# Optimization experiments

Hardware: AMD Instinct MI355X
Metric: run time of the kernel (lower is better)

Reference implementation:

```python
import jax, jax.numpy as jnp
import numpy as np

B = 128        # graph pairs per batch
NPG = 512      # nodes per graph (equal-size graphs -> dense batch is a reshape)
D = 64         # input feature dim
DEG = 16       # avg degree
FILTERS = [64, 32, 16]
RDIM = 10      # resize_dim
CCH = 8        # conv channels per similarity image
MLP = [32, 16, 8, 4, 1]


def _make_edges(rng, n_graphs, npg, deg):
    E = n_graphs * npg * deg
    off = np.repeat(np.arange(n_graphs, dtype=np.int64) * npg, npg * deg)
    src = rng.integers(0, npg, E) + off
    dst = rng.integers(0, npg, E) + off
    return jnp.asarray(np.stack([src, dst]), dtype=jnp.int32)


def setup_inputs() -> dict:
    key = jax.random.key(0)
    ks = jax.random.split(key, 40)
    rng = np.random.default_rng(0)
    N = B * NPG
    inp = {}
    inp['x_i'] = jax.random.normal(ks[0], (N, D), jnp.float32)
    inp['x_j'] = jax.random.normal(ks[1], (N, D), jnp.float32)
    # GCN weights
    dims = [D] + FILTERS
    k = 2
    for li in range(3):
        fi, fo = dims[li], dims[li + 1]
        inp[f'gcn_w{li}'] = jax.random.normal(ks[k], (fi, fo), jnp.float32) / np.sqrt(fi); k += 1
        inp[f'gcn_b{li}'] = jnp.zeros((fo,), jnp.float32)
    # Conv filters: one Conv2d(1->CCH, 3x3, SAME) per GNN layer, OIHW kernels
    for li in range(3):
        inp[f'conv_w{li}'] = jax.random.normal(ks[k], (CCH, 1, 3, 3), jnp.float32) / 3.0; k += 1
        inp[f'conv_b{li}'] = jnp.zeros((CCH,), jnp.float32)
    # MLP (Linear-ReLU stack) + scoring layer
    mdims = [3 * CCH * RDIM * RDIM] + MLP
    for li in range(len(MLP)):
        fi, fo = mdims[li], mdims[li + 1]
        inp[f'mlp_w{li}'] = jax.random.normal(ks[k], (fi, fo), jnp.float32) / np.sqrt(fi); k += 1
        inp[f'mlp_b{li}'] = jnp.zeros((fo,), jnp.float32)
    inp['score_w'] = jax.random.normal(ks[k], (1, 1), jnp.float32); k += 1
    inp['score_b'] = jnp.zeros((1,), jnp.float32)
    # Graph structure (int constants)
    inp['edge_index_i'] = _make_edges(rng, B, NPG, DEG)
    inp['edge_index_j'] = _make_edges(rng, B, NPG, DEG)
    batch = jnp.asarray(np.repeat(np.arange(B, dtype=np.int64), NPG), dtype=jnp.int32)
    inp['batch_i'] = batch
    inp['batch_j'] = batch
    return inp


def _gcn(x, ei, w, b):
    # PyG GCNConv: A_hat = D^-1/2 (A + I) D^-1/2 ; out = A_hat (x W) + b
    src, dst = ei[0], ei[1]
    n = x.shape[0]
    xw = x @ w
    deg = jax.ops.segment_sum(jnp.ones(ei.shape[1], xw.dtype), dst, num_segments=n) + 1.0
    inv = jax.lax.rsqrt(deg)
    msg = xw[src] * (inv[src] * inv[dst])[:, None]
    agg = jax.ops.segment_sum(msg, dst, num_segments=n)
    return agg + xw * (inv * inv)[:, None] + b


def _forward(x_i, x_j, gcn_w0, gcn_b0, gcn_w1, gcn_b1, gcn_w2, gcn_b2,
             conv_w0, conv_b0, conv_w1, conv_b1, conv_w2, conv_b2,
             mlp_w0, mlp_b0, mlp_w1, mlp_b1, mlp_w2, mlp_b2, mlp_w3, mlp_b3, mlp_w4, mlp_b4,
             score_w, score_b, edge_index_i, edge_index_j):
    gws = [(gcn_w0, gcn_b0), (gcn_w1, gcn_b1), (gcn_w2, gcn_b2)]
    cvs = [(conv_w0, conv_b0), (conv_w1, conv_b1), (conv_w2, conv_b2)]
    embs = []
    for li, (w, b) in enumerate(gws):
        x_i = _gcn(x_i, edge_index_i, w, b)
        x_j = _gcn(x_j, edge_index_j, w, b)
        if li != len(gws) - 1:  # activation + dropout (eval mode -> identity)
            x_i = jax.nn.relu(x_i)
            x_j = jax.nn.relu(x_j)
        h_i = x_i.reshape(B, NPG, -1)  # to_dense_batch (equal-size graphs)
        h_j = x_j.reshape(B, NPG, -1)
        sim = jnp.einsum('bnd,bmd->bnm', h_i, h_j)  # [B, NPG, NPG]
        simr = jax.image.resize(sim, (B, RDIM, RDIM), method='bilinear', antialias=False)
        cw, cb = cvs[li]
        y = jax.lax.conv_general_dilated(simr[:, None], cw, (1, 1), 'SAME')
        y = jax.nn.relu(y + cb[None, :, None, None])  # [B, CCH, RDIM, RDIM]
        embs.append(y.reshape(B, -1))
    feat = jnp.concatenate(embs, axis=1)  # [B, 3*CCH*RDIM*RDIM]
    for w, b in [(mlp_w0, mlp_b0), (mlp_w1, mlp_b1), (mlp_w2, mlp_b2), (mlp_w3, mlp_b3), (mlp_w4, mlp_b4)]:
        feat = jax.nn.relu(feat @ w + b)
    score = jax.nn.sigmoid(feat @ score_w + score_b)
    return score.reshape(-1)


def reference(x_i, x_j, gcn_w0, gcn_b0, gcn_w1, gcn_b1, gcn_w2, gcn_b2,
              conv_w0, conv_b0, conv_w1, conv_b1, conv_w2, conv_b2,
              mlp_w0, mlp_b0, mlp_w1, mlp_b1, mlp_w2, mlp_b2, mlp_w3, mlp_b3, mlp_w4, mlp_b4,
              score_w, score_b, edge_index_i, edge_index_j, batch_i, batch_j):
    # batch_i/batch_j are implicit in the block layout (equal-size graphs)
    return _forward(x_i, x_j, gcn_w0, gcn_b0, gcn_w1, gcn_b1, gcn_w2, gcn_b2,
                    conv_w0, conv_b0, conv_w1, conv_b1, conv_w2, conv_b2,
                    mlp_w0, mlp_b0, mlp_w1, mlp_b1, mlp_w2, mlp_b2, mlp_w3, mlp_b3, mlp_w4, mlp_b4,
                    score_w, score_b, edge_index_i, edge_index_j)
```

## Files before the change

### kernel.cpp

```cpp
#include <hip/hip_runtime.h>
#include <hip/hip_fp16.h>

typedef float fvec4 __attribute__((ext_vector_type(4)));
typedef int ivec4 __attribute__((ext_vector_type(4)));

#define NN 65536
#define EE 1048576
#define BB 128
#define NPG 512
#define EPG 8192

__device__ __forceinline__ int pkrtz(float a, float b) {
  union { __half2 h; int i; } u; u.h = __floats2half2_rn(a, b); return u.i;
}
__device__ __forceinline__ float2 up2(int v) {
  union { int i; __half2 h; } u; u.i = v; return __half22float2(u.h);
}

#define ACCQ(SA, SB, w) { float2 f_; \
  f_ = up2((w)[0]); (SA)[0] += f_.x; (SA)[1] += f_.y; \
  f_ = up2((w)[1]); (SA)[2] += f_.x; (SA)[3] += f_.y; \
  f_ = up2((w)[2]); (SB)[0] += f_.x; (SB)[1] += f_.y; \
  f_ = up2((w)[3]); (SB)[2] += f_.x; (SB)[3] += f_.y; }

__global__ __launch_bounds__(512)
void k_all(const float* __restrict__ x_i, const float* __restrict__ x_j,
           const float* __restrict__ gw0, const float* __restrict__ gb0,
           const float* __restrict__ gw1, const float* __restrict__ gb1,
           const float* __restrict__ gw2, const float* __restrict__ gb2,
           const int* __restrict__ ei, const int* __restrict__ ej,
           float* __restrict__ hs0, float* __restrict__ hs1, float* __restrict__ hs2) {
  __shared__ ivec4 bufA[NPG * 4];
  __shared__ ivec4 bufB[NPG * 4];
  __shared__ unsigned short sids[EPG];
  __shared__ int cnt[NPG];
  __shared__ int posb[NPG];
  __shared__ int nodeOf[NPG];
  __shared__ int bins[64];
  __shared__ int binpos[64];
  __shared__ int wsum[8];
  unsigned short* const dsts = reinterpret_cast<unsigned short*>(bufA);

  const int side = blockIdx.x >> 7;
  const int g = blockIdx.x & 127;
  const float* __restrict__ x = side ? x_j : x_i;
  const int* __restrict__ eidx = side ? ej : ei;
  const int v = threadIdx.x;
  const int base = g * NPG;
  const int ebase = g * EPG;

  cnt[v] = 0;
  if (v < 64) bins[v] = 0;
  __syncthreads();
  for (int k = v; k < EPG; k += 512) {
    int d = eidx[EE + ebase + k] - base;
    dsts[k] = (unsigned short)d;
    atomicAdd(&cnt[d], 1);
  }
  __syncthreads();

  const int count = cnt[v];
  const int deg = count > 63 ? 63 : count;
  atomicAdd(&bins[deg], 1);
  int xa = count;
  const int lane = v & 63;
#pragma unroll
  for (int d = 1; d < 64; d <<= 1) {
    int y = __shfl_up(xa, d, 64);
    if (lane >= d) xa += y;
  }
  const int wid = v >> 6;
  if (lane == 63) wsum[wid] = xa;
  __syncthreads();
  if (v < 64) {
    if (v == 0) {
      int a = 0;
#pragma unroll
      for (int i = 0; i < 8; ++i) { int tv = wsum[i]; wsum[i] = a; a += tv; }
    }
    int c = bins[v];
    int xb = c;
#pragma unroll
    for (int d = 1; d < 64; d <<= 1) {
      int y = __shfl_up(xb, d, 64);
      if (v >= d) xb += y;
    }
    binpos[v] = xb - c;
  }
  __syncthreads();
  const int start_v = xa - count + wsum[wid];
  posb[v] = start_v;
  {
    int rank = atomicAdd(&binpos[deg], 1);
    nodeOf[rank] = v;
  }
  __syncthreads();

  for (int k = v; k < EPG; k += 512) {
    int lv = eidx[ebase + k] - base;
    int p = atomicAdd(&posb[dsts[k]], 1);
    sids[p] = (unsigned short)((lv << 2) | ((lv >> 1) & 3));
  }
  __syncthreads();

  const int node = nodeOf[v];
  const int ncount = cnt[node];
  const int nstart = posb[node] - ncount;
  const float inv_v = rsqrtf((float)ncount + 1.0f);
  const int myKey = (node << 2) | ((node >> 1) & 3);

  constexpr int srows[20] = {25, 26, 76, 77, 127, 128, 178, 179, 229, 230,
                             281, 282, 332, 333, 383, 384, 434, 435, 485, 486};
  int slot = -1;
#pragma unroll
  for (int i = 0; i < 20; ++i)
    if (node == srows[i]) slot = i;
  const int hb = (side * BB + g) * 20;

  fvec4 a0[16];
#pragma unroll
  for (int q = 0; q < 16; ++q) a0[q] = fvec4{0.f, 0.f, 0.f, 0.f};
  {
    const fvec4* xv = reinterpret_cast<const fvec4*>(x + (size_t)(base + node) * 64);
#pragma unroll 1
    for (int k16 = 0; k16 < 4; ++k16) {
      fvec4 xq[4];
#pragma unroll
      for (int u = 0; u < 4; ++u) xq[u] = xv[4 * k16 + u];
#pragma unroll
      for (int u = 0; u < 4; ++u) {
#pragma unroll
        for (int j = 0; j < 4; ++j) {
          const float xk = xq[u][j];
          const fvec4* wr = reinterpret_cast<const fvec4*>(gw0 + (size_t)(16 * k16 + 4 * u + j) * 64);
#pragma unroll
          for (int q = 0; q < 16; ++q) a0[q] += xk * wr[q];
        }
      }
    }
  }

  fvec4 s[8];
#pragma unroll
  for (int q = 0; q < 8; ++q) s[q] = a0[q] * inv_v;
#pragma unroll
  for (int q_ = 0; q_ < 4; ++q_) {
    ivec4 w_;
    w_[0] = pkrtz(s[2 * q_][0], s[2 * q_][1]);
    w_[1] = pkrtz(s[2 * q_][2], s[2 * q_][3]);
    w_[2] = pkrtz(s[2 * q_ + 1][0], s[2 * q_ + 1][1]);
    w_[3] = pkrtz(s[2 * q_ + 1][2], s[2 * q_ + 1][3]);
    bufA[myKey ^ q_] = w_;
  }
  __syncthreads();

  {
    const int end = nstart + ncount;
    for (int e = nstart; e < end; ++e) {
      const int K = sids[e];
      const ivec4 w0 = bufA[K], w1 = bufA[K ^ 1], w2 = bufA[K ^ 2], w3 = bufA[K ^ 3];
      ACCQ(s[0], s[1], w0) ACCQ(s[2], s[3], w1) ACCQ(s[4], s[5], w2) ACCQ(s[6], s[7], w3)
    }
  }

  fvec4 sB[8];
#pragma unroll
  for (int q = 0; q < 8; ++q) sB[q] = a0[8 + q] * inv_v;
#pragma unroll
  for (int q_ = 0; q_ < 4; ++q_) {
    ivec4 w_;
    w_[0] = pkrtz(sB[2 * q_][0], sB[2 * q_][1]);
    w_[1] = pkrtz(sB[2 * q_][2], sB[2 * q_][3]);
    w_[2] = pkrtz(sB[2 * q_ + 1][0], sB[2 * q_ + 1][1]);
    w_[3] = pkrtz(sB[2 * q_ + 1][2], sB[2 * q_ + 1][3]);
    bufB[myKey ^ q_] = w_;
  }

  fvec4 y1[8];
#pragma unroll
  for (int p = 0; p < 8; ++p) y1[p] = fvec4{0.f, 0.f, 0.f, 0.f};
  {
    const fvec4* gb0v = reinterpret_cast<const fvec4*>(gb0);
    fvec4* hp = reinterpret_cast<fvec4*>(hs0 + ((size_t)hb + slot) * 64);
#pragma unroll
    for (int q = 0; q < 8; ++q) {
      fvec4 o = s[q] * inv_v + gb0v[q];
#pragma unroll
      for (int j = 0; j < 4; ++j) o[j] = fmaxf(o[j], 0.f);
      if (slot >= 0) hp[q] = o;
#pragma unroll
      for (int j = 0; j < 4; ++j) {
        const float hf = o[j];
        const fvec4* wr = reinterpret_cast<const fvec4*>(gw1 + (size_t)(q * 4 + j) * 32);
#pragma unroll
        for (int p = 0; p < 8; ++p) y1[p] += hf * wr[p];
      }
    }
  }
  __syncthreads();

  {
    const int end = nstart + ncount;
    for (int e = nstart; e < end; ++e) {
      const int K = sids[e];
      const ivec4 w0 = bufB[K], w1 = bufB[K ^ 1], w2 = bufB[K ^ 2], w3 = bufB[K ^ 3];
      ACCQ(sB[0], sB[1], w0) ACCQ(sB[2], sB[3], w1) ACCQ(sB[4], sB[5], w2) ACCQ(sB[6], sB[7], w3)
    }
  }
  {
    const fvec4* gb0v = reinterpret_cast<const fvec4*>(gb0);
    fvec4* hp = reinterpret_cast<fvec4*>(hs0 + ((size_t)hb + slot) * 64);
#pragma unroll
    for (int q = 0; q < 8; ++q) {
      fvec4 o = sB[q] * inv_v + gb0v[8 + q];
#pragma unroll
      for (int j = 0; j < 4; ++j) o[j] = fmaxf(o[j], 0.f);
      if (slot >= 0) hp[8 + q] = o;
#pragma unroll
      for (int j = 0; j < 4; ++j) {
        const float hf = o[j];
        const fvec4* wr = reinterpret_cast<const fvec4*>(gw1 + (size_t)((8 + q) * 4 + j) * 32);
#pragma unroll
        for (int p = 0; p < 8; ++p) y1[p] += hf * wr[p];
      }
    }
  }

  fvec4 s1[8];
#pragma unroll
  for (int q = 0; q < 8; ++q) s1[q] = y1[q] * inv_v;
#pragma unroll
  for (int q_ = 0; q_ < 4; ++q_) {
    ivec4 w_;
    w_[0] = pkrtz(s1[2 * q_][0], s1[2 * q_][1]);
    w_[1] = pkrtz(s1[2 * q_][2], s1[2 * q_][3]);
    w_[2] = pkrtz(s1[2 * q_ + 1][0], s1[2 * q_ + 1][1]);
    w_[3] = pkrtz(s1[2 * q_ + 1][2], s1[2 * q_ + 1][3]);
    bufA[myKey ^ q_] = w_;
  }
  __syncthreads();

  {
    const int end = nstart + ncount;
    for (int e = nstart; e < end; ++e) {
      const int K = sids[e];
      const ivec4 w0 = bufA[K], w1 = bufA[K ^ 1], w2 = bufA[K ^ 2], w3 = bufA[K ^ 3];
      ACCQ(s1[0], s1[1], w0) ACCQ(s1[2], s1[3], w1) ACCQ(s1[4], s1[5], w2) ACCQ(s1[6], s1[7], w3)
    }
  }
  fvec4 y2[4];
#pragma unroll
  for (int p = 0; p < 4; ++p) y2[p] = fvec4{0.f, 0.f, 0.f, 0.f};
  {
    const fvec4* gb1v = reinterpret_cast<const fvec4*>(gb1);
    fvec4* hp = reinterpret_cast<fvec4*>(hs1 + ((size_t)hb + slot) * 32);
#pragma unroll
    for (int q = 0; q < 8; ++q) {
      fvec4 o = s1[q] * inv_v + gb1v[q];
#pragma unroll
      for (int j = 0; j < 4; ++j) o[j] = fmaxf(o[j], 0.f);
      if (slot >= 0) hp[q] = o;
#pragma unroll
      for (int j = 0; j < 4; ++j) {
        const float hf = o[j];
        const fvec4* wr = reinterpret_cast<const fvec4*>(gw2 + (size_t)(q * 4 + j) * 16);
#pragma unroll
        for (int p = 0; p < 4; ++p) y2[p] += hf * wr[p];
      }
    }
  }

  fvec4 s2[4];
#pragma unroll
  for (int q = 0; q < 4; ++q) s2[q] = y2[q] * inv_v;
  {
    ivec4 w0, w1;
    w0[0] = pkrtz(s2[0][0], s2[0][1]); w0[1] = pkrtz(s2[0][2], s2[0][3]);
    w0[2] = pkrtz(s2[1][0], s2[1][1]); w0[3] = pkrtz(s2[1][2], s2[1][3]);
    w1[0] = pkrtz(s2[2][0], s2[2][1]); w1[1] = pkrtz(s2[2][2], s2[2][3]);
    w1[2] = pkrtz(s2[3][0], s2[3][1]); w1[3] = pkrtz(s2[3][2], s2[3][3]);
    bufB[myKey] = w0;
    bufB[myKey ^ 1] = w1;
  }
  __syncthreads();

  if (slot >= 0) {
    const int end = nstart + ncount;
    for (int e = nstart; e < end; ++e) {
      const int K = sids[e];
      const ivec4 w0 = bufB[K], w1 = bufB[K ^ 1];
      ACCQ(s2[0], s2[1], w0) ACCQ(s2[2], s2[3], w1)
    }
    const fvec4* gb2v = reinterpret_cast<const fvec4*>(gb2);
    fvec4* hp = reinterpret_cast<fvec4*>(hs2 + ((size_t)hb + slot) * 16);
#pragma unroll
    for (int q = 0; q < 4; ++q) hp[q] = s2[q] * inv_v + gb2v[q];
  }
}

__global__ __launch_bounds__(256) void k_head(const float* __restrict__ hs0, const float* __restrict__ hs1,
                                              const float* __restrict__ hs2,
                                              const float* __restrict__ cw0, const float* __restrict__ cb0,
                                              const float* __restrict__ cw1, const float* __restrict__ cb1,
                                              const float* __restrict__ cw2, const float* __restrict__ cb2,
                                              const float* __restrict__ mw0, const float* __restrict__ mb0,
                                              const float* __restrict__ mw1, const float* __restrict__ mb1,
                                              const float* __restrict__ mw2, const float* __restrict__ mb2,
                                              const float* __restrict__ mw3, const float* __restrict__ mb3,
                                              const float* __restrict__ mw4, const float* __restrict__ mb4,
                                              const float* __restrict__ sw, const float* __restrict__ sb,
                                              float* __restrict__ out) {
  __shared__ float hi[2240];
  __shared__ float hj[2240];
  __shared__ float sim[400];
  __shared__ float simr[100];
  __shared__ float feat[2400];
  __shared__ float red[256];
  __shared__ float mbuf[60];
  const int b = blockIdx.x, t = threadIdx.x;

  for (int k = t; k < 1280; k += 256) {
    hi[k] = hs0[(size_t)(0 * BB + b) * 1280 + k];
    hj[k] = hs0[(size_t)(1 * BB + b) * 1280 + k];
  }
  for (int k = t; k < 640; k += 256) {
    hi[1280 + k] = hs1[(size_t)(0 * BB + b) * 640 + k];
    hj[1280 + k] = hs1[(size_t)(1 * BB + b) * 640 + k];
  }
  for (int k = t; k < 320; k += 256) {
    hi[1920 + k] = hs2[(size_t)(0 * BB + b) * 320 + k];
    hj[1920 + k] = hs2[(size_t)(1 * BB + b) * 320 + k];
  }
  __syncthreads();

  const int Fs[3] = {64, 32, 16};
  const int HOFF[3] = {0, 1280, 1920};
  const float* CW[3] = {cw0, cw1, cw2};
  const float* CB[3] = {cb0, cb1, cb2};

  for (int li = 0; li < 3; ++li) {
    const int F = Fs[li];
    const float* Hi = hi + HOFF[li];
    const float* Hj = hj + HOFF[li];
    for (int p = t; p < 400; p += 256) {
      int r = p / 20, cq = p % 20;
      float a = 0.0f;
      for (int d = 0; d < F; ++d) a += Hi[r * F + d] * Hj[cq * F + d];
      sim[p] = a;
    }
    __syncthreads();
    if (t < 100) {
      int oy = t / 10, ox = t % 10;
      float cy = (oy + 0.5f) * (512.0f / 10.0f) - 0.5f;
      float cx = (ox + 0.5f) * (512.0f / 10.0f) - 0.5f;
      float fy = cy - floorf(cy);
      float fx = cx - floorf(cx);
      int r0 = 2 * oy, c0 = 2 * ox;
      float s00 = sim[r0 * 20 + c0], s01 = sim[r0 * 20 + c0 + 1];
      float s10 = sim[(r0 + 1) * 20 + c0], s11 = sim[(r0 + 1) * 20 + c0 + 1];
      simr[t] = (1.0f - fy) * ((1.0f - fx) * s00 + fx * s01) + fy * ((1.0f - fx) * s10 + fx * s11);
    }
    __syncthreads();
    const float* cw = CW[li];
    const float* cb = CB[li];
    for (int idx = t; idx < 800; idx += 256) {
      int cch = idx / 100, rem = idx % 100, y = rem / 10, x = rem % 10;
      float a = cb[cch];
#pragma unroll
      for (int ky = 0; ky < 3; ++ky) {
#pragma unroll
        for (int kx = 0; kx < 3; ++kx) {
          int iy = y + ky - 1, ix = x + kx - 1;
          if (iy >= 0 && iy < 10 && ix >= 0 && ix < 10)
            a += cw[cch * 9 + ky * 3 + kx] * simr[iy * 10 + ix];
        }
      }
      feat[li * 800 + idx] = fmaxf(a, 0.0f);
    }
    __syncthreads();
  }

  {
    int f = t & 31, part = t >> 5;
    float a = 0.0f;
    int k0 = part * 300;
    for (int k = k0; k < k0 + 300; ++k) a += feat[k] * mw0[k * 32 + f];
    red[t] = a;
    __syncthreads();
    if (t < 32) {
      float s = mb0[t];
#pragma unroll
      for (int p = 0; p < 8; ++p) s += red[p * 32 + t];
      mbuf[t] = fmaxf(s, 0.0f);
    }
    __syncthreads();
  }
  if (t < 16) {
    float s = mb1[t];
    for (int k = 0; k < 32; ++k) s += mbuf[k] * mw1[k * 16 + t];
    mbuf[32 + t] = fmaxf(s, 0.0f);
  }
  __syncthreads();
  if (t < 8) {
    float s = mb2[t];
    for (int k = 0; k < 16; ++k) s += mbuf[32 + k] * mw2[k * 8 + t];
    mbuf[48 + t] = fmaxf(s, 0.0f);
  }
  __syncthreads();
  if (t < 4) {
    float s = mb3[t];
    for (int k = 0; k < 8; ++k) s += mbuf[48 + k] * mw3[k * 4 + t];
    mbuf[56 + t] = fmaxf(s, 0.0f);
  }
  __syncthreads();
  if (t == 0) {
    float s = mb4[0];
    for (int k = 0; k < 4; ++k) s += mbuf[56 + k] * mw4[k];
    s = fmaxf(s, 0.0f);
    float z = s * sw[0] + sb[0];
    out[b] = 1.0f / (1.0f + expf(-z));
  }
}

extern "C" void kernel_launch(void* const* d_in, const int* in_sizes, int n_in,
                              void* d_out, int out_size, void* d_ws, size_t ws_size,
                              hipStream_t stream) {
  (void)in_sizes; (void)n_in; (void)out_size; (void)ws_size;
  const float* x_i = (const float*)d_in[0];
  const float* x_j = (const float*)d_in[1];
  const float* gw0 = (const float*)d_in[2];
  const float* gb0 = (const float*)d_in[3];
  const float* gw1 = (const float*)d_in[4];
  const float* gb1 = (const float*)d_in[5];
  const float* gw2 = (const float*)d_in[6];
  const float* gb2 = (const float*)d_in[7];
  const float* cw0 = (const float*)d_in[8];
  const float* cb0 = (const float*)d_in[9];
  const float* cw1 = (const float*)d_in[10];
  const float* cb1 = (const float*)d_in[11];
  const float* cw2 = (const float*)d_in[12];
  const float* cb2 = (const float*)d_in[13];
  const float* mw0 = (const float*)d_in[14];
  const float* mb0 = (const float*)d_in[15];
  const float* mw1 = (const float*)d_in[16];
  const float* mb1 = (const float*)d_in[17];
  const float* mw2 = (const float*)d_in[18];
  const float* mb2 = (const float*)d_in[19];
  const float* mw3 = (const float*)d_in[20];
  const float* mb3 = (const float*)d_in[21];
  const float* mw4 = (const float*)d_in[22];
  const float* mb4 = (const float*)d_in[23];
  const float* scw = (const float*)d_in[24];
  const float* scb = (const float*)d_in[25];
  const int* ei = (const int*)d_in[26];
  const int* ej = (const int*)d_in[27];
  float* out = (float*)d_out;

  char* p = (char*)d_ws;
  auto take = [&](size_t bytes) {
    char* r = p;
    p += (bytes + 255) & ~(size_t)255;
    return r;
  };
  float* hs0 = (float*)take((size_t)2 * BB * 20 * 64 * 4);
  float* hs1 = (float*)take((size_t)2 * BB * 20 * 32 * 4);
  float* hs2 = (float*)take((size_t)2 * BB * 20 * 16 * 4);

  k_all<<<2 * BB, 512, 0, stream>>>(x_i, x_j, gw0, gb0, gw1, gb1, gw2, gb2,
                                    ei, ej, hs0, hs1, hs2);
  k_head<<<BB, 256, 0, stream>>>(hs0, hs1, hs2, cw0, cb0, cw1, cb1, cw2, cb2,
                                 mw0, mb0, mw1, mb1, mw2, mb2, mw3, mb3, mw4, mb4,
                                 scw, scb, out);
}
```

Before: 131.7 us.

## Merge layer-0 half buffers into one sync, unroll gathers, spread final-layer rows

```diff
diff --git a/kernel.cpp b/kernel.cpp
--- a/kernel.cpp
+++ b/kernel.cpp
@@ -22,6 +22,21 @@
   f_ = up2((w)[1]); (SA)[2] += f_.x; (SA)[3] += f_.y; \
   f_ = up2((w)[2]); (SB)[0] += f_.x; (SB)[1] += f_.y; \
   f_ = up2((w)[3]); (SB)[2] += f_.x; (SB)[3] += f_.y; }
+
+#define GATHER32(buf, S, startE, countE) { \
+  int e_ = (startE); const int end_ = (startE) + (countE); \
+  for (; e_ + 2 <= end_; e_ += 2) { \
+    const int Ka_ = sids[e_], Kb_ = sids[e_ + 1]; \
+    const ivec4 a0_ = (buf)[Ka_], a1_ = (buf)[Ka_ ^ 1], a2_ = (buf)[Ka_ ^ 2], a3_ = (buf)[Ka_ ^ 3]; \
+    const ivec4 b0_ = (buf)[Kb_], b1_ = (buf)[Kb_ ^ 1], b2_ = (buf)[Kb_ ^ 2], b3_ = (buf)[Kb_ ^ 3]; \
+    ACCQ((S)[0], (S)[1], a0_) ACCQ((S)[2], (S)[3], a1_) ACCQ((S)[4], (S)[5], a2_) ACCQ((S)[6], (S)[7], a3_) \
+    ACCQ((S)[0], (S)[1], b0_) ACCQ((S)[2], (S)[3], b1_) ACCQ((S)[4], (S)[5], b2_) ACCQ((S)[6], (S)[7], b3_) \
+  } \
+  if (e_ < end_) { \
+    const int Ka_ = sids[e_]; \
+    const ivec4 a0_ = (buf)[Ka_], a1_ = (buf)[Ka_ ^ 1], a2_ = (buf)[Ka_ ^ 2], a3_ = (buf)[Ka_ ^ 3]; \
+    ACCQ((S)[0], (S)[1], a0_) ACCQ((S)[2], (S)[3], a1_) ACCQ((S)[4], (S)[5], a2_) ACCQ((S)[6], (S)[7], a3_) \
+  } }
 
 __global__ __launch_bounds__(512)
 void k_all(const float* __restrict__ x_i, const float* __restrict__ x_j,
@@ -145,36 +160,21 @@
   for (int q = 0; q < 8; ++q) s[q] = a0[q] * inv_v;
 #pragma unroll
   for (int q_ = 0; q_ < 4; ++q_) {
-    ivec4 w_;
-    w_[0] = pkrtz(s[2 * q_][0], s[2 * q_][1]);
-    w_[1] = pkrtz(s[2 * q_][2], s[2 * q_][3]);
-    w_[2] = pkrtz(s[2 * q_ + 1][0], s[2 * q_ + 1][1]);
-    w_[3] = pkrtz(s[2 * q_ + 1][2], s[2 * q_ + 1][3]);
-    bufA[myKey ^ q_] = w_;
-  }
-  __syncthreads();
-
-  {
-    const int end = nstart + ncount;
-    for (int e = nstart; e < end; ++e) {
-      const int K = sids[e];
-      const ivec4 w0 = bufA[K], w1 = bufA[K ^ 1], w2 = bufA[K ^ 2], w3 = bufA[K ^ 3];
-      ACCQ(s[0], s[1], w0) ACCQ(s[2], s[3], w1) ACCQ(s[4], s[5], w2) ACCQ(s[6], s[7], w3)
-    }
-  }
-
-  fvec4 sB[8];
-#pragma unroll
-  for (int q = 0; q < 8; ++q) sB[q] = a0[8 + q] * inv_v;
-#pragma unroll
-  for (int q_ = 0; q_ < 4; ++q_) {
-    ivec4 w_;
-    w_[0] = pkrtz(sB[2 * q_][0], sB[2 * q_][1]);
-    w_[1] = pkrtz(sB[2 * q_][2], sB[2 * q_][3]);
-    w_[2] = pkrtz(sB[2 * q_ + 1][0], sB[2 * q_ + 1][1]);
-    w_[3] = pkrtz(sB[2 * q_ + 1][2], sB[2 * q_ + 1][3]);
-    bufB[myKey ^ q_] = w_;
-  }
+    ivec4 wA, wB;
+    wA[0] = pkrtz(s[2 * q_][0], s[2 * q_][1]);
+    wA[1] = pkrtz(s[2 * q_][2], s[2 * q_][3]);
+    wA[2] = pkrtz(s[2 * q_ + 1][0], s[2 * q_ + 1][1]);
+    wA[3] = pkrtz(s[2 * q_ + 1][2], s[2 * q_ + 1][3]);
+    fvec4 b0 = a0[8 + 2 * q_] * inv_v;
+    fvec4 b1 = a0[8 + 2 * q_ + 1] * inv_v;
+    wB[0] = pkrtz(b0[0], b0[1]); wB[1] = pkrtz(b0[2], b0[3]);
+    wB[2] = pkrtz(b1[0], b1[1]); wB[3] = pkrtz(b1[2], b1[3]);
+    bufA[myKey ^ q_] = wA;
+    bufB[myKey ^ q_] = wB;
+  }
+  __syncthreads();
+
+  GATHER32(bufA, s, nstart, ncount)
 
   fvec4 y1[8];
 #pragma unroll
@@ -197,16 +197,16 @@
       }
     }
   }
-  __syncthreads();
-
-  {
-    const int end = nstart + ncount;
-    for (int e = nstart; e < end; ++e) {
-      const int K = sids[e];
-      const ivec4 w0 = bufB[K], w1 = bufB[K ^ 1], w2 = bufB[K ^ 2], w3 = bufB[K ^ 3];
-      ACCQ(sB[0], sB[1], w0) ACCQ(sB[2], sB[3], w1) ACCQ(sB[4], sB[5], w2) ACCQ(sB[6], sB[7], w3)
-    }
-  }
+
+  fvec4 sB[8];
+#pragma unroll
+  for (int q = 0; q < 8; ++q) sB[q] = fvec4{0.f, 0.f, 0.f, 0.f};
+  {
+    const ivec4 w0 = bufB[myKey], w1 = bufB[myKey ^ 1], w2 = bufB[myKey ^ 2], w3 = bufB[myKey ^ 3];
+    ACCQ(sB[0], sB[1], w0) ACCQ(sB[2], sB[3], w1) ACCQ(sB[4], sB[5], w2) ACCQ(sB[6], sB[7], w3)
+  }
+  GATHER32(bufB, sB, nstart, ncount)
+
   {
     const fvec4* gb0v = reinterpret_cast<const fvec4*>(gb0);
     fvec4* hp = reinterpret_cast<fvec4*>(hs0 + ((size_t)hb + slot) * 64);
@@ -225,6 +225,7 @@
       }
     }
   }
+  __syncthreads();
 
   fvec4 s1[8];
 #pragma unroll
@@ -240,14 +241,8 @@
   }
   __syncthreads();
 
-  {
-    const int end = nstart + ncount;
-    for (int e = nstart; e < end; ++e) {
-      const int K = sids[e];
-      const ivec4 w0 = bufA[K], w1 = bufA[K ^ 1], w2 = bufA[K ^ 2], w3 = bufA[K ^ 3];
-      ACCQ(s1[0], s1[1], w0) ACCQ(s1[2], s1[3], w1) ACCQ(s1[4], s1[5], w2) ACCQ(s1[6], s1[7], w3)
-    }
-  }
+  GATHER32(bufA, s1, nstart, ncount)
+
   fvec4 y2[4];
 #pragma unroll
   for (int p = 0; p < 4; ++p) y2[p] = fvec4{0.f, 0.f, 0.f, 0.f};
@@ -270,31 +265,49 @@
     }
   }
 
-  fvec4 s2[4];
-#pragma unroll
-  for (int q = 0; q < 4; ++q) s2[q] = y2[q] * inv_v;
-  {
+  {
+    fvec4 q0 = y2[0] * inv_v, q1 = y2[1] * inv_v, q2 = y2[2] * inv_v, q3 = y2[3] * inv_v;
     ivec4 w0, w1;
-    w0[0] = pkrtz(s2[0][0], s2[0][1]); w0[1] = pkrtz(s2[0][2], s2[0][3]);
-    w0[2] = pkrtz(s2[1][0], s2[1][1]); w0[3] = pkrtz(s2[1][2], s2[1][3]);
-    w1[0] = pkrtz(s2[2][0], s2[2][1]); w1[1] = pkrtz(s2[2][2], s2[2][3]);
-    w1[2] = pkrtz(s2[3][0], s2[3][1]); w1[3] = pkrtz(s2[3][2], s2[3][3]);
+    w0[0] = pkrtz(q0[0], q0[1]); w0[1] = pkrtz(q0[2], q0[3]);
+    w0[2] = pkrtz(q1[0], q1[1]); w0[3] = pkrtz(q1[2], q1[3]);
+    w1[0] = pkrtz(q2[0], q2[1]); w1[1] = pkrtz(q2[2], q2[3]);
+    w1[2] = pkrtz(q3[0], q3[1]); w1[3] = pkrtz(q3[2], q3[3]);
     bufB[myKey] = w0;
     bufB[myKey ^ 1] = w1;
   }
   __syncthreads();
 
-  if (slot >= 0) {
-    const int end = nstart + ncount;
-    for (int e = nstart; e < end; ++e) {
-      const int K = sids[e];
-      const ivec4 w0 = bufB[K], w1 = bufB[K ^ 1];
+  if (v < 20) {
+    const int n = srows[v];
+    const int ccount = cnt[n];
+    const int cstart = posb[n] - ccount;
+    const float cinv = rsqrtf((float)ccount + 1.0f);
+    const int ckey = (n << 2) | ((n >> 1) & 3);
+    fvec4 s2[4];
+#pragma unroll
+    for (int q = 0; q < 4; ++q) s2[q] = fvec4{0.f, 0.f, 0.f, 0.f};
+    {
+      const ivec4 w0 = bufB[ckey], w1 = bufB[ckey ^ 1];
       ACCQ(s2[0], s2[1], w0) ACCQ(s2[2], s2[3], w1)
     }
+    int e = cstart;
+    const int end = cstart + ccount;
+    for (; e + 2 <= end; e += 2) {
+      const int Ka = sids[e], Kb = sids[e + 1];
+      const ivec4 a0_ = bufB[Ka], a1_ = bufB[Ka ^ 1];
+      const ivec4 b0_ = bufB[Kb], b1_ = bufB[Kb ^ 1];
+      ACCQ(s2[0], s2[1], a0_) ACCQ(s2[2], s2[3], a1_)
+      ACCQ(s2[0], s2[1], b0_) ACCQ(s2[2], s2[3], b1_)
+    }
+    if (e < end) {
+      const int Ka = sids[e];
+      const ivec4 a0_ = bufB[Ka], a1_ = bufB[Ka ^ 1];
+      ACCQ(s2[0], s2[1], a0_) ACCQ(s2[2], s2[3], a1_)
+    }
     const fvec4* gb2v = reinterpret_cast<const fvec4*>(gb2);
-    fvec4* hp = reinterpret_cast<fvec4*>(hs2 + ((size_t)hb + slot) * 16);
-#pragma unroll
-    for (int q = 0; q < 4; ++q) hp[q] = s2[q] * inv_v + gb2v[q];
+    fvec4* hp = reinterpret_cast<fvec4*>(hs2 + ((size_t)hb + v) * 16);
+#pragma unroll
+    for (int q = 0; q < 4; ++q) hp[q] = s2[q] * cinv + gb2v[q];
   }
 }
 
```

Result: no change. 130.3 us (-1.0%).

## Split fused GCN kernel into three per-layer kernels with feature-half blocks

Applied to the files above, without the earlier changes.

```diff
diff --git a/kernel.cpp b/kernel.cpp
--- a/kernel.cpp
+++ b/kernel.cpp
@@ -23,34 +23,42 @@
   f_ = up2((w)[2]); (SB)[0] += f_.x; (SB)[1] += f_.y; \
   f_ = up2((w)[3]); (SB)[2] += f_.x; (SB)[3] += f_.y; }
 
+__device__ __forceinline__ int slot_of(int node) {
+  constexpr int srows[20] = {25, 26, 76, 77, 127, 128, 178, 179, 229, 230,
+                             281, 282, 332, 333, 383, 384, 434, 435, 485, 486};
+  int slot = -1;
+#pragma unroll
+  for (int i = 0; i < 20; ++i)
+    if (node == srows[i]) slot = i;
+  return slot;
+}
+__constant__ int c_srows[20] = {25, 26, 76, 77, 127, 128, 178, 179, 229, 230,
+                                281, 282, 332, 333, 383, 384, 434, 435, 485, 486};
+
 __global__ __launch_bounds__(512)
-void k_all(const float* __restrict__ x_i, const float* __restrict__ x_j,
-           const float* __restrict__ gw0, const float* __restrict__ gb0,
-           const float* __restrict__ gw1, const float* __restrict__ gb1,
-           const float* __restrict__ gw2, const float* __restrict__ gb2,
-           const int* __restrict__ ei, const int* __restrict__ ej,
-           float* __restrict__ hs0, float* __restrict__ hs1, float* __restrict__ hs2) {
-  __shared__ ivec4 bufA[NPG * 4];
-  __shared__ ivec4 bufB[NPG * 4];
+void kA(const float* __restrict__ x_i, const float* __restrict__ x_j,
+        const float* __restrict__ gw0, const float* __restrict__ gb0,
+        const float* __restrict__ gw1,
+        const int* __restrict__ ei, const int* __restrict__ ej,
+        unsigned short* __restrict__ sidsG, unsigned int* __restrict__ packG,
+        float* __restrict__ hs0, unsigned int* __restrict__ y1G) {
+  __shared__ ivec4 buf[NPG * 4];
   __shared__ unsigned short sids[EPG];
   __shared__ int cnt[NPG];
   __shared__ int posb[NPG];
-  __shared__ int nodeOf[NPG];
-  __shared__ int bins[64];
-  __shared__ int binpos[64];
   __shared__ int wsum[8];
-  unsigned short* const dsts = reinterpret_cast<unsigned short*>(bufA);
-
-  const int side = blockIdx.x >> 7;
-  const int g = blockIdx.x & 127;
+  unsigned short* const dsts = reinterpret_cast<unsigned short*>(buf);
+
+  const int bid = blockIdx.x;
+  const int half = bid & 1;
+  const int sg = bid >> 1;
+  const int side = sg >> 7, g = sg & 127;
   const float* __restrict__ x = side ? x_j : x_i;
   const int* __restrict__ eidx = side ? ej : ei;
   const int v = threadIdx.x;
-  const int base = g * NPG;
-  const int ebase = g * EPG;
+  const int base = g * NPG, ebase = g * EPG;
 
   cnt[v] = 0;
-  if (v < 64) bins[v] = 0;
   __syncthreads();
   for (int k = v; k < EPG; k += 512) {
     int d = eidx[EE + ebase + k] - base;
@@ -60,8 +68,6 @@
   __syncthreads();
 
   const int count = cnt[v];
-  const int deg = count > 63 ? 63 : count;
-  atomicAdd(&bins[deg], 1);
   int xa = count;
   const int lane = v & 63;
 #pragma unroll
@@ -72,56 +78,27 @@
   const int wid = v >> 6;
   if (lane == 63) wsum[wid] = xa;
   __syncthreads();
-  if (v < 64) {
-    if (v == 0) {
-      int a = 0;
-#pragma unroll
-      for (int i = 0; i < 8; ++i) { int tv = wsum[i]; wsum[i] = a; a += tv; }
-    }
-    int c = bins[v];
-    int xb = c;
-#pragma unroll
-    for (int d = 1; d < 64; d <<= 1) {
-      int y = __shfl_up(xb, d, 64);
-      if (v >= d) xb += y;
-    }
-    binpos[v] = xb - c;
-  }
-  __syncthreads();
-  const int start_v = xa - count + wsum[wid];
-  posb[v] = start_v;
-  {
-    int rank = atomicAdd(&binpos[deg], 1);
-    nodeOf[rank] = v;
-  }
+  if (v == 0) {
+    int a = 0;
+#pragma unroll
+    for (int i = 0; i < 8; ++i) { int tv = wsum[i]; wsum[i] = a; a += tv; }
+  }
+  __syncthreads();
+  posb[v] = xa - count + wsum[wid];
   __syncthreads();
 
   for (int k = v; k < EPG; k += 512) {
     int lv = eidx[ebase + k] - base;
     int p = atomicAdd(&posb[dsts[k]], 1);
-    sids[p] = (unsigned short)((lv << 2) | ((lv >> 1) & 3));
-  }
-  __syncthreads();
-
-  const int node = nodeOf[v];
-  const int ncount = cnt[node];
-  const int nstart = posb[node] - ncount;
-  const float inv_v = rsqrtf((float)ncount + 1.0f);
-  const int myKey = (node << 2) | ((node >> 1) & 3);
-
-  constexpr int srows[20] = {25, 26, 76, 77, 127, 128, 178, 179, 229, 230,
-                             281, 282, 332, 333, 383, 384, 434, 435, 485, 486};
-  int slot = -1;
-#pragma unroll
-  for (int i = 0; i < 20; ++i)
-    if (node == srows[i]) slot = i;
-  const int hb = (side * BB + g) * 20;
-
-  fvec4 a0[16];
-#pragma unroll
-  for (int q = 0; q < 16; ++q) a0[q] = fvec4{0.f, 0.f, 0.f, 0.f};
-  {
-    const fvec4* xv = reinterpret_cast<const fvec4*>(x + (size_t)(base + node) * 64);
+    sids[p] = (unsigned short)lv;
+  }
+
+  fvec4 a0[8];
+#pragma unroll
+  for (int q = 0; q < 8; ++q) a0[q] = fvec4{0.f, 0.f, 0.f, 0.f};
+  {
+    const fvec4* xv = reinterpret_cast<const fvec4*>(x + (size_t)(base + v) * 64);
+    const float* w0h = gw0 + half * 32;
 #pragma unroll 1
     for (int k16 = 0; k16 < 4; ++k16) {
       fvec4 xq[4];
@@ -132,14 +109,24 @@
 #pragma unroll
         for (int j = 0; j < 4; ++j) {
           const float xk = xq[u][j];
-          const fvec4* wr = reinterpret_cast<const fvec4*>(gw0 + (size_t)(16 * k16 + 4 * u + j) * 64);
-#pragma unroll
-          for (int q = 0; q < 16; ++q) a0[q] += xk * wr[q];
+          const fvec4* wr = reinterpret_cast<const fvec4*>(w0h + (size_t)(16 * k16 + 4 * u + j) * 64);
+#pragma unroll
+          for (int q = 0; q < 8; ++q) a0[q] += xk * wr[q];
         }
       }
     }
   }
-
+  __syncthreads();
+
+  const int sgE = sg * EPG;
+  if (half == 0) {
+    const int* srcI = reinterpret_cast<const int*>(sids);
+    int* dstI = reinterpret_cast<int*>(sidsG + sgE);
+    for (int k = v; k < EPG / 2; k += 512) dstI[k] = srcI[k];
+    packG[sg * NPG + v] = ((unsigned int)(posb[v] - count) << 16) | (unsigned int)count;
+  }
+  const float inv_v = rsqrtf((float)count + 1.0f);
+  const int myKey = (v << 2) | ((v >> 1) & 3);
   fvec4 s[8];
 #pragma unroll
   for (int q = 0; q < 8; ++q) s[q] = a0[q] * inv_v;
@@ -150,38 +137,39 @@
     w_[1] = pkrtz(s[2 * q_][2], s[2 * q_][3]);
     w_[2] = pkrtz(s[2 * q_ + 1][0], s[2 * q_ + 1][1]);
     w_[3] = pkrtz(s[2 * q_ + 1][2], s[2 * q_ + 1][3]);
-    bufA[myKey ^ q_] = w_;
-  }
-  __syncthreads();
-
-  {
-    const int end = nstart + ncount;
-    for (int e = nstart; e < end; ++e) {
-      const int K = sids[e];
-      const ivec4 w0 = bufA[K], w1 = bufA[K ^ 1], w2 = bufA[K ^ 2], w3 = bufA[K ^ 3];
-      ACCQ(s[0], s[1], w0) ACCQ(s[2], s[3], w1) ACCQ(s[4], s[5], w2) ACCQ(s[6], s[7], w3)
-    }
-  }
-
-  fvec4 sB[8];
-#pragma unroll
-  for (int q = 0; q < 8; ++q) sB[q] = a0[8 + q] * inv_v;
-#pragma unroll
-  for (int q_ = 0; q_ < 4; ++q_) {
-    ivec4 w_;
-    w_[0] = pkrtz(sB[2 * q_][0], sB[2 * q_][1]);
-    w_[1] = pkrtz(sB[2 * q_][2], sB[2 * q_][3]);
-    w_[2] = pkrtz(sB[2 * q_ + 1][0], sB[2 * q_ + 1][1]);
-    w_[3] = pkrtz(sB[2 * q_ + 1][2], sB[2 * q_ + 1][3]);
-    bufB[myKey ^ q_] = w_;
-  }
-
-  fvec4 y1[8];
-#pragma unroll
-  for (int p = 0; p < 8; ++p) y1[p] = fvec4{0.f, 0.f, 0.f, 0.f};
-  {
-    const fvec4* gb0v = reinterpret_cast<const fvec4*>(gb0);
-    fvec4* hp = reinterpret_cast<fvec4*>(hs0 + ((size_t)hb + slot) * 64);
+    buf[myKey ^ q_] = w_;
+  }
+  __syncthreads();
+
+  const int nstart = posb[v] - count;
+  {
+    int e = nstart;
+    const int end = nstart + count;
+    for (; e + 2 <= end; e += 2) {
+      const int la = sids[e], lb = sids[e + 1];
+      const int Ka = (la << 2) | ((la >> 1) & 3);
+      const int Kb = (lb << 2) | ((lb >> 1) & 3);
+      const ivec4 a0_ = buf[Ka], a1_ = buf[Ka ^ 1], a2_ = buf[Ka ^ 2], a3_ = buf[Ka ^ 3];
+      const ivec4 b0_ = buf[Kb], b1_ = buf[Kb ^ 1], b2_ = buf[Kb ^ 2], b3_ = buf[Kb ^ 3];
+      ACCQ(s[0], s[1], a0_) ACCQ(s[2], s[3], a1_) ACCQ(s[4], s[5], a2_) ACCQ(s[6], s[7], a3_)
+      ACCQ(s[0], s[1], b0_) ACCQ(s[2], s[3], b1_) ACCQ(s[4], s[5], b2_) ACCQ(s[6], s[7], b3_)
+    }
+    if (e < end) {
+      const int la = sids[e];
+      const int Ka = (la << 2) | ((la >> 1) & 3);
+      const ivec4 a0_ = buf[Ka], a1_ = buf[Ka ^ 1], a2_ = buf[Ka ^ 2], a3_ = buf[Ka ^ 3];
+      ACCQ(s[0], s[1], a0_) ACCQ(s[2], s[3], a1_) ACCQ(s[4], s[5], a2_) ACCQ(s[6], s[7], a3_)
+    }
+  }
+
+  const int slot = slot_of(v);
+  const int hb = (side * BB + g) * 20;
+  fvec4 y1P[8];
+#pragma unroll
+  for (int p = 0; p < 8; ++p) y1P[p] = fvec4{0.f, 0.f, 0.f, 0.f};
+  {
+    const fvec4* gb0v = reinterpret_cast<const fvec4*>(gb0 + half * 32);
+    fvec4* hp = reinterpret_cast<fvec4*>(hs0 + ((size_t)hb + slot) * 64 + half * 32);
 #pragma unroll
     for (int q = 0; q < 8; ++q) {
       fvec4 o = s[q] * inv_v + gb0v[q];
@@ -191,110 +179,184 @@
 #pragma unroll
       for (int j = 0; j < 4; ++j) {
         const float hf = o[j];
-        const fvec4* wr = reinterpret_cast<const fvec4*>(gw1 + (size_t)(q * 4 + j) * 32);
-#pragma unroll
-        for (int p = 0; p < 8; ++p) y1[p] += hf * wr[p];
+        const fvec4* wr = reinterpret_cast<const fvec4*>(gw1 + (size_t)(half * 32 + q * 4 + j) * 32);
+#pragma unroll
+        for (int p = 0; p < 8; ++p) y1P[p] += hf * wr[p];
       }
     }
   }
-  __syncthreads();
-
-  {
-    const int end = nstart + ncount;
-    for (int e = nstart; e < end; ++e) {
-      const int K = sids[e];
-      const ivec4 w0 = bufB[K], w1 = bufB[K ^ 1], w2 = bufB[K ^ 2], w3 = bufB[K ^ 3];
-      ACCQ(sB[0], sB[1], w0) ACCQ(sB[2], sB[3], w1) ACCQ(sB[4], sB[5], w2) ACCQ(sB[6], sB[7], w3)
-    }
-  }
-  {
-    const fvec4* gb0v = reinterpret_cast<const fvec4*>(gb0);
-    fvec4* hp = reinterpret_cast<fvec4*>(hs0 + ((size_t)hb + slot) * 64);
-#pragma unroll
-    for (int q = 0; q < 8; ++q) {
-      fvec4 o = sB[q] * inv_v + gb0v[8 + q];
+  {
+    unsigned int* yp = y1G + ((size_t)(sg * 2 + half) * NPG + v) * 16;
+#pragma unroll
+    for (int w = 0; w < 16; ++w)
+      yp[w] = (unsigned int)pkrtz(y1P[w >> 1][(w & 1) * 2], y1P[w >> 1][(w & 1) * 2 + 1]);
+  }
+}
+
+__global__ __launch_bounds__(512)
+void kB(const float* __restrict__ gb1, const float* __restrict__ gw2,
+        const unsigned short* __restrict__ sidsG, const unsigned int* __restrict__ packG,
+        const unsigned int* __restrict__ y1G,
+        float* __restrict__ hs1, unsigned int* __restrict__ y2G) {
+  __shared__ ivec4 buf[NPG * 2];
+  __shared__ unsigned short sids[EPG];
+  const int bid = blockIdx.x;
+  const int half = bid & 1;
+  const int sg = bid >> 1;
+  const int side = sg >> 7, g = sg & 127;
+  const int v = threadIdx.x;
+
+  {
+    const int* srcI = reinterpret_cast<const int*>(sidsG + sg * EPG);
+    int* dstI = reinterpret_cast<int*>(sids);
+    for (int k = v; k < EPG / 2; k += 512) dstI[k] = srcI[k];
+  }
+  const unsigned int pack = packG[sg * NPG + v];
+  const int count = (int)(pack & 0xffffu);
+  const int nstart = (int)(pack >> 16);
+  const float inv_v = rsqrtf((float)count + 1.0f);
+
+  fvec4 s1[4];
+  {
+    const unsigned int* p0 = y1G + ((size_t)(sg * 2 + 0) * NPG + v) * 16 + half * 8;
+    const unsigned int* p1 = y1G + ((size_t)(sg * 2 + 1) * NPG + v) * 16 + half * 8;
+#pragma unroll
+    for (int w = 0; w < 8; ++w) {
+      float2 fa = up2((int)p0[w]);
+      float2 fb = up2((int)p1[w]);
+      s1[w >> 1][(w & 1) * 2] = (fa.x + fb.x) * inv_v;
+      s1[w >> 1][(w & 1) * 2 + 1] = (fa.y + fb.y) * inv_v;
+    }
+  }
+  __syncthreads();
+  const int myKey = (v << 1) | (v & 1);
+  {
+    ivec4 w0, w1;
+    w0[0] = pkrtz(s1[0][0], s1[0][1]); w0[1] = pkrtz(s1[0][2], s1[0][3]);
+    w0[2] = pkrtz(s1[1][0], s1[1][1]); w0[3] = pkrtz(s1[1][2], s1[1][3]);
+    w1[0] = pkrtz(s1[2][0], s1[2][1]); w1[1] = pkrtz(s1[2][2], s1[2][3]);
+    w1[2] = pkrtz(s1[3][0], s1[3][1]); w1[3] = pkrtz(s1[3][2], s1[3][3]);
+    buf[myKey] = w0;
+    buf[myKey ^ 1] = w1;
+  }
+  __syncthreads();
+
+  {
+    int e = nstart;
+    const int end = nstart + count;
+    for (; e + 2 <= end; e += 2) {
+      const int la = sids[e], lb = sids[e + 1];
+      const int Ka = (la << 1) | (la & 1), Kb = (lb << 1) | (lb & 1);
+      const ivec4 a0_ = buf[Ka], a1_ = buf[Ka ^ 1];
+      const ivec4 b0_ = buf[Kb], b1_ = buf[Kb ^ 1];
+      ACCQ(s1[0], s1[1], a0_) ACCQ(s1[2], s1[3], a1_)
+      ACCQ(s1[0], s1[1], b0_) ACCQ(s1[2], s1[3], b1_)
+    }
+    if (e < end) {
+      const int la = sids[e];
+      const int Ka = (la << 1) | (la & 1);
+      const ivec4 a0_ = buf[Ka], a1_ = buf[Ka ^ 1];
+      ACCQ(s1[0], s1[1], a0_) ACCQ(s1[2], s1[3], a1_)
+    }
+  }
+
+  const int slot = slot_of(v);
+  const int hb = (side * BB + g) * 20;
+  fvec4 y2P[4];
+#pragma unroll
+  for (int p = 0; p < 4; ++p) y2P[p] = fvec4{0.f, 0.f, 0.f, 0.f};
+  {
+    const fvec4* gb1v = reinterpret_cast<const fvec4*>(gb1 + half * 16);
+    fvec4* hp = reinterpret_cast<fvec4*>(hs1 + ((size_t)hb + slot) * 32 + half * 16);
+#pragma unroll
+    for (int q = 0; q < 4; ++q) {
+      fvec4 o = s1[q] * inv_v + gb1v[q];
 #pragma unroll
       for (int j = 0; j < 4; ++j) o[j] = fmaxf(o[j], 0.f);
-      if (slot >= 0) hp[8 + q] = o;
+      if (slot >= 0) hp[q] = o;
 #pragma unroll
       for (int j = 0; j < 4; ++j) {
         const float hf = o[j];
-        const fvec4* wr = reinterpret_cast<const fvec4*>(gw1 + (size_t)((8 + q) * 4 + j) * 32);
-#pragma unroll
-        for (int p = 0; p < 8; ++p) y1[p] += hf * wr[p];
+        const fvec4* wr = reinterpret_cast<const fvec4*>(gw2 + (size_t)(half * 16 + q * 4 + j) * 16);
+#pragma unroll
+        for (int p = 0; p < 4; ++p) y2P[p] += hf * wr[p];
       }
     }
   }
-
-  fvec4 s1[8];
-#pragma unroll
-  for (int q = 0; q < 8; ++q) s1[q] = y1[q] * inv_v;
-#pragma unroll
-  for (int q_ = 0; q_ < 4; ++q_) {
-    ivec4 w_;
-    w_[0] = pkrtz(s1[2 * q_][0], s1[2 * q_][1]);
-    w_[1] = pkrtz(s1[2 * q_][2], s1[2 * q_][3]);
-    w_[2] = pkrtz(s1[2 * q_ + 1][0], s1[2 * q_ + 1][1]);
-    w_[3] = pkrtz(s1[2 * q_ + 1][2], s1[2 * q_ + 1][3]);
-    bufA[myKey ^ q_] = w_;
-  }
-  __syncthreads();
-
-  {
-    const int end = nstart + ncount;
-    for (int e = nstart; e < end; ++e) {
-      const int K = sids[e];
-      const ivec4 w0 = bufA[K], w1 = bufA[K ^ 1], w2 = bufA[K ^ 2], w3 = bufA[K ^ 3];
-      ACCQ(s1[0], s1[1], w0) ACCQ(s1[2], s1[3], w1) ACCQ(s1[4], s1[5], w2) ACCQ(s1[6], s1[7], w3)
-    }
-  }
-  fvec4 y2[4];
-#pragma unroll
-  for (int p = 0; p < 4; ++p) y2[p] = fvec4{0.f, 0.f, 0.f, 0.f};
-  {
-    const fvec4* gb1v = reinterpret_cast<const fvec4*>(gb1);
-    fvec4* hp = reinterpret_cast<fvec4*>(hs1 + ((size_t)hb + slot) * 32);
-#pragma unroll
-    for (int q = 0; q < 8; ++q) {
-      fvec4 o = s1[q] * inv_v + gb1v[q];
-#pragma unroll
-      for (int j = 0; j < 4; ++j) o[j] = fmaxf(o[j], 0.f);
-      if (slot >= 0) hp[q] = o;
-#pragma unroll
-      for (int j = 0; j < 4; ++j) {
-        const float hf = o[j];
-        const fvec4* wr = reinterpret_cast<const fvec4*>(gw2 + (size_t)(q * 4 + j) * 16);
-#pragma unroll
-        for (int p = 0; p < 4; ++p) y2[p] += hf * wr[p];
-      }
-    }
-  }
-
-  fvec4 s2[4];
-#pragma unroll
-  for (int q = 0; q < 4; ++q) s2[q] = y2[q] * inv_v;
-  {
+  {
+    unsigned int* yp = y2G + ((size_t)(sg * 2 + half) * NPG + v) * 8;
+#pragma unroll
+    for (int w = 0; w < 8; ++w)
+      yp[w] = (unsigned int)pkrtz(y2P[w >> 1][(w & 1) * 2], y2P[w >> 1][(w & 1) * 2 + 1]);
+  }
+}
+
+__global__ __launch_bounds__(512)
+void kC(const float* __restrict__ gb2,
+        const unsigned short* __restrict__ sidsG, const unsigned int* __restrict__ packG,
+        const unsigned int* __restrict__ y2G, float* __restrict__ hs2) {
+  __shared__ ivec4 buf[NPG * 2];
+  __shared__ unsigned short sids[EPG];
+  const int sg = blockIdx.x;
+  const int side = sg >> 7, g = sg & 127;
+  const int v = threadIdx.x;
+
+  {
+    const int* srcI = reinterpret_cast<const int*>(sidsG + sg * EPG);
+    int* dstI = reinterpret_cast<int*>(sids);
+    for (int k = v; k < EPG / 2; k += 512) dstI[k] = srcI[k];
+  }
+  const unsigned int pack = packG[sg * NPG + v];
+  const int count = (int)(pack & 0xffffu);
+  const float inv_v = rsqrtf((float)count + 1.0f);
+
+  const int myKey = (v << 1) | (v & 1);
+  {
+    const unsigned int* p0 = y2G + ((size_t)(sg * 2 + 0) * NPG + v) * 8;
+    const unsigned int* p1 = y2G + ((size_t)(sg * 2 + 1) * NPG + v) * 8;
+    fvec4 y2[4];
+#pragma unroll
+    for (int w = 0; w < 8; ++w) {
+      float2 fa = up2((int)p0[w]);
+      float2 fb = up2((int)p1[w]);
+      y2[w >> 1][(w & 1) * 2] = (fa.x + fb.x) * inv_v;
+      y2[w >> 1][(w & 1) * 2 + 1] = (fa.y + fb.y) * inv_v;
+    }
     ivec4 w0, w1;
-    w0[0] = pkrtz(s2[0][0], s2[0][1]); w0[1] = pkrtz(s2[0][2], s2[0][3]);
-    w0[2] = pkrtz(s2[1][0], s2[1][1]); w0[3] = pkrtz(s2[1][2], s2[1][3]);
-    w1[0] = pkrtz(s2[2][0], s2[2][1]); w1[1] = pkrtz(s2[2][2], s2[2][3]);
-    w1[2] = pkrtz(s2[3][0], s2[3][1]); w1[3] = pkrtz(s2[3][2], s2[3][3]);
-    bufB[myKey] = w0;
-    bufB[myKey ^ 1] = w1;
-  }
-  __syncthreads();
-
-  if (slot >= 0) {
-    const int end = nstart + ncount;
-    for (int e = nstart; e < end; ++e) {
-      const int K = sids[e];
-      const ivec4 w0 = bufB[K], w1 = bufB[K ^ 1];
+    w0[0] = pkrtz(y2[0][0], y2[0][1]); w0[1] = pkrtz(y2[0][2], y2[0][3]);
+    w0[2] = pkrtz(y2[1][0], y2[1][1]); w0[3] = pkrtz(y2[1][2], y2[1][3]);
+    w1[0] = pkrtz(y2[2][0], y2[2][1]); w1[1] = pkrtz(y2[2][2], y2[2][3]);
+    w1[2] = pkrtz(y2[3][0], y2[3][1]); w1[3] = pkrtz(y2[3][2], y2[3][3]);
+    buf[myKey] = w0;
+    buf[myKey ^ 1] = w1;
+  }
+  __syncthreads();
+
+  if (v < 20) {
+    const int n = c_srows[v];
+    const unsigned int cp = packG[sg * NPG + n];
+    const int ccount = (int)(cp & 0xffffu);
+    const int cstart = (int)(cp >> 16);
+    const float cinv = rsqrtf((float)ccount + 1.0f);
+    const int ckey = (n << 1) | (n & 1);
+    fvec4 s2[4];
+#pragma unroll
+    for (int q = 0; q < 4; ++q) s2[q] = fvec4{0.f, 0.f, 0.f, 0.f};
+    {
+      const ivec4 w0 = buf[ckey], w1 = buf[ckey ^ 1];
       ACCQ(s2[0], s2[1], w0) ACCQ(s2[2], s2[3], w1)
     }
+    for (int e = cstart; e < cstart + ccount; ++e) {
+      const int la = sids[e];
+      const int Ka = (la << 1) | (la & 1);
+      const ivec4 w0 = buf[Ka], w1 = buf[Ka ^ 1];
+      ACCQ(s2[0], s2[1], w0) ACCQ(s2[2], s2[3], w1)
+    }
+    const int hb = (side * BB + g) * 20;
     const fvec4* gb2v = reinterpret_cast<const fvec4*>(gb2);
-    fvec4* hp = reinterpret_cast<fvec4*>(hs2 + ((size_t)hb + slot) * 16);
-#pragma unroll
-    for (int q = 0; q < 4; ++q) hp[q] = s2[q] * inv_v + gb2v[q];
+    fvec4* hp = reinterpret_cast<fvec4*>(hs2 + ((size_t)hb + v) * 16);
+#pragma unroll
+    for (int q = 0; q < 4; ++q) hp[q] = s2[q] * cinv + gb2v[q];
   }
 }
 
@@ -465,9 +527,15 @@
   float* hs0 = (float*)take((size_t)2 * BB * 20 * 64 * 4);
   float* hs1 = (float*)take((size_t)2 * BB * 20 * 32 * 4);
   float* hs2 = (float*)take((size_t)2 * BB * 20 * 16 * 4);
-
-  k_all<<<2 * BB, 512, 0, stream>>>(x_i, x_j, gw0, gb0, gw1, gb1, gw2, gb2,
-                                    ei, ej, hs0, hs1, hs2);
+  unsigned short* sidsG = (unsigned short*)take((size_t)2 * BB * EPG * 2);
+  unsigned int* packG = (unsigned int*)take((size_t)2 * BB * NPG * 4);
+  unsigned int* y1G = (unsigned int*)take((size_t)2 * BB * 2 * NPG * 16 * 4);
+  unsigned int* y2G = (unsigned int*)take((size_t)2 * BB * 2 * NPG * 8 * 4);
+
+  kA<<<2 * BB * 2, 512, 0, stream>>>(x_i, x_j, gw0, gb0, gw1, ei, ej,
+                                     sidsG, packG, hs0, y1G);
+  kB<<<2 * BB * 2, 512, 0, stream>>>(gb1, gw2, sidsG, packG, y1G, hs1, y2G);
+  kC<<<2 * BB, 512, 0, stream>>>(gb2, sidsG, packG, y2G, hs2);
   k_head<<<BB, 256, 0, stream>>>(hs0, hs1, hs2, cw0, cb0, cw1, cb1, cw2, cb2,
                                  mw0, mb0, mw1, mb1, mw2, mb2, mw3, mb3, mw4, mb4,
                                  scw, scb, out);
```

After: 121.6 us. 7.6% less time.
